# Kernel optimization log

Hardware: AMD Instinct MI355X
Metric: run time of the kernel (lower is better)

The kernel has to match this reference:

```python
import jax, jax.numpy as jnp
import numpy as np
import math

ESM_DIM = 1280

def setup_inputs() -> dict:
    key = jax.random.key(0)
    ks = jax.random.split(key, 12)
    B, Ls, Lc, D = 16, 1024, 2048, ESM_DIM
    scale = 0.02
    return {
        "cyclase": jax.random.normal(ks[0], (B, Lc, D), jnp.float32),
        "substrate": jax.random.normal(ks[1], (B, Ls, D), jnp.float32),
        "cyclase_mask": jnp.ones((B, Lc), jnp.float32),
        "substrate_mask": jnp.ones((B, Ls), jnp.float32),
        "Wq": jax.random.uniform(ks[2], (D, D), jnp.float32) * scale,
        "Wk": jax.random.uniform(ks[3], (D, D), jnp.float32) * scale,
        "Wv": jax.random.uniform(ks[4], (D, D), jnp.float32) * scale,
        "W1": jax.random.normal(ks[5], (2 * D, 512), jnp.float32) * scale,
        "b1": jnp.zeros((512,), jnp.float32),
        "W2": jax.random.normal(ks[6], (512, 64), jnp.float32) * scale,
        "b2": jnp.zeros((64,), jnp.float32),
        "W3": jax.random.normal(ks[7], (64, 1), jnp.float32) * scale,
        "b3": jnp.zeros((1,), jnp.float32),
    }


def reference(cyclase, substrate, cyclase_mask, substrate_mask,
              Wq, Wk, Wv, W1, b1, W2, b2, W3, b3):
    # Cross attention: substrate is the query, cyclase is key/value.
    q = jnp.einsum('bsd,de->bse', substrate, Wq)   # [B,Ls,D]
    k = jnp.einsum('bcd,de->bce', cyclase, Wk)     # [B,Lc,D]
    v = jnp.einsum('bcd,de->bce', cyclase, Wv)     # [B,Lc,D]
    scores = jnp.einsum('bse,bce->bsc', q, k) / math.sqrt(q.shape[-1])
    # NOTE: original torch code masks `attn_scores` but softmaxes
    # `scaled_attn_scores`, so the padding mask has no effect. Replicated.
    weights = jax.nn.softmax(scores, axis=-1)      # [B,Ls,Lc]
    attn_out = jnp.einsum('bsc,bce->bse', weights, v)  # [B,Ls,D]
    x1_avg = jnp.mean(attn_out, axis=1)            # [B,D]
    sub_avg = jnp.mean(substrate, axis=1)          # [B,D]
    x = jnp.concatenate([x1_avg, sub_avg], axis=1) # [B,2D]
    h = jax.nn.relu(x @ W1 + b1)
    h = jax.nn.relu(h @ W2 + b2)
    return jax.nn.sigmoid(h @ W3 + b3)             # [B,1]
```

## Files before the change

### kernel.cpp

```cpp
#include <hip/hip_runtime.h>
#include <hip/hip_bf16.h>

#define DEV static __device__ __forceinline__

typedef __attribute__((ext_vector_type(16))) float f32x16;
typedef __attribute__((ext_vector_type(8)))  short bf16x8;

#if defined(__has_builtin)
#  if __has_builtin(__builtin_amdgcn_cvt_pk_fp8_f32) && __has_builtin(__builtin_amdgcn_cvt_f32_fp8)
#    define HW_FP8 1
#  endif
#endif

DEV ushort f2bf(float f){
  union { float f; unsigned u; } v; v.f = f;
  return (ushort)((v.u + 0x7FFFu + ((v.u >> 16) & 1u)) >> 16);
}
DEV float bf2f(ushort u){
  union { unsigned u; float f; } v; v.u = ((unsigned)u) << 16;
  return v.f;
}

DEV unsigned char f2e4m3_sw(float f){
  union { float f; unsigned u; } v; v.f = f;
  unsigned s = (v.u >> 24) & 0x80;
  float a = fabsf(f);
  if (a >= 448.f) return s | 0x7E;
  if (a < 0.0009765625f) return (unsigned char)s;
  if (a < 0.015625f) {
    int m = (int)rintf(a * 512.f);
    return (unsigned char)(s | (m >= 8 ? 8 : m));
  }
  unsigned ab = v.u & 0x7FFFFFFF;
  unsigned r = ab + 0x0007FFFF + ((ab >> 20) & 1);
  unsigned e = (r >> 23) - 127 + 7;
  unsigned m = (r >> 20) & 7;
  if (e > 15 || (e == 15 && m > 6)) return s | 0x7E;
  return (unsigned char)(s | (e << 3) | m);
}
DEV float e4m32f_sw(unsigned char c){
  unsigned e = (c >> 3) & 15, m = c & 7;
  float v;
  if (e) { union { unsigned u; float f; } w; w.u = ((e + 120u) << 23) | (m << 20); v = w.f; }
  else v = (float)m * 0.001953125f;
  return (c & 0x80) ? -v : v;
}

DEV unsigned pack4_fp8(float a, float b, float c, float d){
#ifdef HW_FP8
  int v = __builtin_amdgcn_cvt_pk_fp8_f32(a, b, 0, false);
  v = __builtin_amdgcn_cvt_pk_fp8_f32(c, d, v, true);
  return (unsigned)v;
#else
  return (unsigned)f2e4m3_sw(a) | ((unsigned)f2e4m3_sw(b) << 8)
       | ((unsigned)f2e4m3_sw(c) << 16) | ((unsigned)f2e4m3_sw(d) << 24);
#endif
}
DEV unsigned char enc_fp8(float a){
#ifdef HW_FP8
  return (unsigned char)(__builtin_amdgcn_cvt_pk_fp8_f32(a, a, 0, false) & 0xFF);
#else
  return f2e4m3_sw(a);
#endif
}
template<int SEL>
DEV float dec_fp8(unsigned u){
#ifdef HW_FP8
  return __builtin_amdgcn_cvt_f32_fp8((int)u, SEL);
#else
  return e4m32f_sw((u >> (SEL * 8)) & 0xFF);
#endif
}

DEV void gload16(const void* g, void* l) {
  __builtin_amdgcn_global_load_lds(
      (const __attribute__((address_space(1))) unsigned*)g,
      (__attribute__((address_space(3))) unsigned*)l, 16, 0, 0);
}

__global__ __launch_bounds__(256)
void cvt_wqk(const float* __restrict__ Wq, const float* __restrict__ Wk,
             ushort* __restrict__ Wq16, ushort* __restrict__ Wk16)
{
  const float* src = blockIdx.y ? Wk : Wq;
  ushort* dst = blockIdx.y ? Wk16 : Wq16;
  const long n8 = 1280l * 1280 / 8;
  const long stride = (long)gridDim.x * 256;
  for (long i = (long)blockIdx.x * 256 + threadIdx.x; i < n8; i += stride) {
    const float4 a = *(const float4*)(src + i * 8);
    const float4 b = *(const float4*)(src + i * 8 + 4);
    union { ushort u[8]; uint4 v; } pk;
    pk.u[0] = f2bf(a.x); pk.u[1] = f2bf(a.y); pk.u[2] = f2bf(a.z); pk.u[3] = f2bf(a.w);
    pk.u[4] = f2bf(b.x); pk.u[5] = f2bf(b.y); pk.u[6] = f2bf(b.z); pk.u[7] = f2bf(b.w);
    *(uint4*)(dst + i * 8) = pk.v;
  }
}

__global__ __launch_bounds__(256)
void cyccvt(const float* __restrict__ cyc, unsigned* __restrict__ cyc8w,
            float* __restrict__ gsum)
{
  const int lane = threadIdx.x & 63, wid = threadIdx.x >> 6;
  const long row = (long)blockIdx.x * 4 + wid;
  const float* src = cyc + row * 1280;
  unsigned* dst = cyc8w + row * 320;
  float s = 0.f;
  #pragma unroll
  for (int i = 0; i < 5; i++) {
    const int d = i * 256 + lane * 4;
    const float4 v = *(const float4*)(src + d);
    s += v.x + v.y + v.z + v.w;
    dst[d >> 2] = pack4_fp8(v.x * 16.f, v.y * 16.f, v.z * 16.f, v.w * 16.f);
  }
  #pragma unroll
  for (int o = 1; o < 64; o <<= 1) s += __shfl_xor(s, o);
  if (lane == 0) gsum[row] = s;
}

__global__ __launch_bounds__(256)
void subprep(const float* __restrict__ sub, const float* __restrict__ mcol,
             unsigned* __restrict__ sub8w, float* __restrict__ tbar)
{
  __shared__ float mc[1280];
  for (int i = threadIdx.x; i < 1280; i += 256) mc[i] = mcol[i];
  __syncthreads();
  const int lane = threadIdx.x & 63, wid = threadIdx.x >> 6;
  const long row = (long)blockIdx.x * 4 + wid;
  const float4* sp = (const float4*)(sub + row * 1280);
  unsigned* dp = sub8w + row * 320;
  float d = 0.f;
  #pragma unroll
  for (int i = 0; i < 5; i++) {
    const int c = i * 64 + lane;
    const float4 v = sp[c];
    d += v.x * mc[c * 4] + v.y * mc[c * 4 + 1] + v.z * mc[c * 4 + 2] + v.w * mc[c * 4 + 3];
    dp[c] = pack4_fp8(v.x * 16.f, v.y * 16.f, v.z * 16.f, v.w * 16.f);
  }
  #pragma unroll
  for (int o = 1; o < 64; o <<= 1) d += __shfl_xor(d, o);
  if (lane == 0) tbar[row] = d;
}

__global__ __launch_bounds__(512, 4)
void gemm_mkq(const ushort* __restrict__ A, const ushort* __restrict__ B,
              ushort* __restrict__ C, int K, int N, int nbx, float scale,
              float* __restrict__ mcol)
{
  __shared__ __align__(16) ushort As[4][4][128][8];
  __shared__ __align__(16) ushort Bs[4][4][128][8];
  const int tid = threadIdx.x, lane = tid & 63, wid = tid >> 6;
  const int wr = wid >> 2, wc = wid & 3;
  const int bx = blockIdx.x % nbx, by = blockIdx.x / nbx;
  const int bm = by * 128, bn = bx * 128;

  f32x16 acc[2];
  #pragma unroll
  for (int i = 0; i < 2; i++)
    #pragma unroll
    for (int e = 0; e < 16; e++) acc[i][e] = 0.f;

  const int kbA = wid >> 1, rqA = wid & 1;
  const ushort* agp = A + (long)(bm + rqA * 64 + lane) * K + kbA * 8;
  const ushort* bgp = B + (long)(bn + rqA * 64 + lane) * K + kbA * 8;
  auto STAGE = [&](int g, int rg) {
    gload16(agp + g * 32, &As[rg][kbA][rqA * 64][0]);
    gload16(bgp + g * 32, &Bs[rg][kbA][rqA * 64][0]);
  };
  const int NG = K >> 5;
  STAGE(0, 0); STAGE(1, 1);
  asm volatile("s_waitcnt vmcnt(2)" ::: "memory");
  __builtin_amdgcn_s_barrier();
  const int lkh = lane >> 5, lr = lane & 31;
  auto GROUP = [&](int g, int rg, int rg2) {
    bf16x8 av[2][2], bv[2];
    #pragma unroll
    for (int kf = 0; kf < 2; kf++) {
      #pragma unroll
      for (int mi = 0; mi < 2; mi++)
        av[mi][kf] = *(const bf16x8*)&As[rg][kf * 2 + lkh][wr * 64 + mi * 32 + lr][0];
      bv[kf] = *(const bf16x8*)&Bs[rg][kf * 2 + lkh][wc * 32 + lr][0];
    }
    if (g + 2 < NG) STAGE(g + 2, rg2);
    __builtin_amdgcn_s_barrier();
    __builtin_amdgcn_s_setprio(1);
    #pragma unroll
    for (int mi = 0; mi < 2; mi++)
      #pragma unroll
      for (int kf = 0; kf < 2; kf++)
        acc[mi] = __builtin_amdgcn_mfma_f32_32x32x16_bf16(av[mi][kf], bv[kf], acc[mi], 0, 0, 0);
    __builtin_amdgcn_s_setprio(0);
    if (g + 2 < NG)      asm volatile("s_waitcnt vmcnt(2)" ::: "memory");
    else if (g + 1 < NG) asm volatile("s_waitcnt vmcnt(0)" ::: "memory");
    __builtin_amdgcn_s_barrier();
  };
  for (int g = 0; g < NG; g += 4) {
    GROUP(g, 0, 2); GROUP(g + 1, 1, 3); GROUP(g + 2, 2, 0); GROUP(g + 3, 3, 1);
  }
  float csum = 0.f;
  #pragma unroll
  for (int mi = 0; mi < 2; mi++)
    #pragma unroll
    for (int rr = 0; rr < 16; rr++) {
      const int row = bm + wr * 64 + mi * 32 + (rr & 3) + 8 * (rr >> 2) + 4 * lkh;
      const int col = bn + wc * 32 + lr;
      const float v = acc[mi][rr] * scale;
      csum += v;
      C[(long)row * N + col] = f2bf(v);
    }
  atomicAdd(&mcol[bn + wc * 32 + lr], csum * (1.f / 1280.f));
}

__global__ __launch_bounds__(320)
void m2cvt(const ushort* __restrict__ Mkq, const float* __restrict__ mcol,
           unsigned* __restrict__ M2w)
{
  const int j = blockIdx.x;
  const int d = threadIdx.x * 4;
  const ushort* mr = Mkq + (long)j * 1280 + d;
  const float* mc = mcol + d;
  M2w[j * 320 + threadIdx.x] = pack4_fp8(
      (bf2f(mr[0]) - mc[0]) * 524288.f, (bf2f(mr[1]) - mc[1]) * 524288.f,
      (bf2f(mr[2]) - mc[2]) * 524288.f, (bf2f(mr[3]) - mc[3]) * 524288.f);
}

template<int MODE, bool BY_FAST>
__global__ __launch_bounds__(512, 2)
void gemm_f8(const unsigned char* __restrict__ A, const unsigned char* __restrict__ B,
             void* __restrict__ Cv, int K, int N, int nbx, int nby,
             long sA, long sB, long sC,
             const float* __restrict__ tbar, const float* __restrict__ gsum)
{
  __shared__ __align__(16) unsigned char As[4][4][256][16];
  __shared__ __align__(16) unsigned char Bs[4][4][256][16];
  const int tid = threadIdx.x, lane = tid & 63, wid = tid >> 6;
  const int wr = wid >> 2, wc = wid & 3;

  const int nwg = gridDim.x;
  const int q = nwg >> 3, r = nwg & 7;
  const int xcd = blockIdx.x & 7, lid = blockIdx.x >> 3;
  const int id = (xcd < r ? xcd * (q + 1) : r * (q + 1) + (xcd - r) * q) + lid;
  const int per = nbx * nby;
  const int z = id / per, rem = id - z * per;
  const int bx = BY_FAST ? rem / nby : rem % nbx;
  const int by = BY_FAST ? rem % nby : rem / nbx;
  const int bm = by * 256, bn = bx * 256;
  const long Ab = (long)z * sA, Bb = (long)z * sB, Cb = (long)z * sC;

  f32x16 acc[4][2];
  #pragma unroll
  for (int i = 0; i < 4; i++)
    #pragma unroll
    for (int j = 0; j < 2; j++)
      #pragma unroll
      for (int e = 0; e < 16; e++) acc[i][j][e] = 0.f;

  const int c0 = wid * 2, c1 = wid * 2 + 1;
  const int kb0 = c0 >> 2, rq0 = c0 & 3, kb1 = c1 >> 2, rq1 = c1 & 3;
  const unsigned char* ag0 = A + Ab + (long)(bm + rq0 * 64 + lane) * K + kb0 * 16;
  const unsigned char* ag1 = A + Ab + (long)(bm + rq1 * 64 + lane) * K + kb1 * 16;
  const unsigned char* bg0 = B + Bb + (long)(bn + rq0 * 64 + lane) * K + kb0 * 16;
  const unsigned char* bg1 = B + Bb + (long)(bn + rq1 * 64 + lane) * K + kb1 * 16;
  auto STAGE_A = [&](int g, int rg) {
    gload16(ag0 + g * 64, &As[rg][kb0][rq0 * 64][0]);
    gload16(ag1 + g * 64, &As[rg][kb1][rq1 * 64][0]);
  };
  auto STAGE_B = [&](int g, int rg) {
    gload16(bg0 + g * 64, &Bs[rg][kb0][rq0 * 64][0]);
    gload16(bg1 + g * 64, &Bs[rg][kb1][rq1 * 64][0]);
  };

  const int NG = K >> 6;
  STAGE_A(0, 0); STAGE_B(0, 0); STAGE_A(1, 1); STAGE_B(1, 1);
  asm volatile("s_waitcnt vmcnt(4)" ::: "memory");
  __builtin_amdgcn_s_barrier();

  const int lkh = lane >> 5, lr = lane & 31;

  auto GROUP = [&](int g, int rg, int rg2) {
    const bool pre = (g + 2 < NG);
    long av[2][4], bv[2][4];
    #pragma unroll
    for (int kf = 0; kf < 4; kf++) {
      #pragma unroll
      for (int mi = 0; mi < 2; mi++)
        av[mi][kf] = *(const long*)&As[rg][kf][wr * 128 + mi * 32 + lr][lkh * 8];
      #pragma unroll
      for (int ni = 0; ni < 2; ni++)
        bv[ni][kf] = *(const long*)&Bs[rg][kf][wc * 64 + ni * 32 + lr][lkh * 8];
    }
    if (pre) STAGE_A(g + 2, rg2);
    __builtin_amdgcn_s_barrier();
    __builtin_amdgcn_s_setprio(1);
    #pragma unroll
    for (int kf = 0; kf < 4; kf++)
      #pragma unroll
      for (int mi = 0; mi < 2; mi++)
        #pragma unroll
        for (int ni = 0; ni < 2; ni++)
          acc[mi][ni] = __builtin_amdgcn_mfma_f32_32x32x16_fp8_fp8(av[mi][kf], bv[ni][kf], acc[mi][ni], 0, 0, 0);
    __builtin_amdgcn_s_setprio(0);
    __builtin_amdgcn_s_barrier();
    #pragma unroll
    for (int kf = 0; kf < 4; kf++)
      #pragma unroll
      for (int mi = 0; mi < 2; mi++)
        av[mi][kf] = *(const long*)&As[rg][kf][wr * 128 + (mi + 2) * 32 + lr][lkh * 8];
    if (pre) STAGE_B(g + 2, rg2);
    __builtin_amdgcn_s_barrier();
    __builtin_amdgcn_s_setprio(1);
    #pragma unroll
    for (int kf = 0; kf < 4; kf++)
      #pragma unroll
      for (int mi = 0; mi < 2; mi++)
        #pragma unroll
        for (int ni = 0; ni < 2; ni++)
          acc[mi + 2][ni] = __builtin_amdgcn_mfma_f32_32x32x16_fp8_fp8(av[mi][kf], bv[ni][kf], acc[mi + 2][ni], 0, 0, 0);
    __builtin_amdgcn_s_setprio(0);
    if (pre)             asm volatile("s_waitcnt vmcnt(4)" ::: "memory");
    else if (g + 1 < NG) asm volatile("s_waitcnt vmcnt(0)" ::: "memory");
    __builtin_amdgcn_s_barrier();
  };

  for (int g = 0; g < NG; g += 4) {
    GROUP(g, 0, 2); GROUP(g + 1, 1, 3); GROUP(g + 2, 2, 0); GROUP(g + 3, 3, 1);
  }

  #pragma unroll
  for (int mi = 0; mi < 4; mi++)
    #pragma unroll
    for (int ni = 0; ni < 2; ni++)
      #pragma unroll
      for (int rr = 0; rr < 16; rr++) {
        const int row = bm + wr * 128 + mi * 32 + (rr & 3) + 8 * (rr >> 2) + 4 * lkh;
        const int col = bn + wc * 64 + ni * 32 + lr;
        if constexpr (MODE == 0) {
          const float v = acc[mi][ni][rr] * 0x1p-16f
                        + tbar[(long)z * 1024 + row] * gsum[(long)z * 2048 + col];
          ((ushort*)Cv)[Cb + (long)row * N + col] = f2bf(v);
        } else {
          ((unsigned char*)Cv)[Cb + (long)row * N + col] = enc_fp8(acc[mi][ni][rr] * 0x1p-11f);
        }
      }
}

__global__ __launch_bounds__(512, 4)
void gemm_f8_128(const unsigned char* __restrict__ A, const unsigned char* __restrict__ B,
                 unsigned char* __restrict__ C, int K, int N, int nbx)
{
  __shared__ __align__(16) unsigned char As[4][4][128][16];
  __shared__ __align__(16) unsigned char Bs[4][4][128][16];
  const int tid = threadIdx.x, lane = tid & 63, wid = tid >> 6;
  const int wr = wid >> 2, wc = wid & 3;

  const int nwg = gridDim.x;
  const int q = nwg >> 3, r = nwg & 7;
  const int xcd = blockIdx.x & 7, lid = blockIdx.x >> 3;
  const int id = (xcd < r ? xcd * (q + 1) : r * (q + 1) + (xcd - r) * q) + lid;
  const int bx = id % nbx, by = id / nbx;
  const int bm = by * 128, bn = bx * 128;

  f32x16 acc[2];
  #pragma unroll
  for (int i = 0; i < 2; i++)
    #pragma unroll
    for (int e = 0; e < 16; e++) acc[i][e] = 0.f;

  const int kbA = wid >> 1, rhA = wid & 1;
  const unsigned char* agp = A + (long)(bm + rhA * 64 + lane) * K + kbA * 16;
  const unsigned char* bgp = B + (long)(bn + rhA * 64 + lane) * K + kbA * 16;
  auto STAGE = [&](int g, int rg) {
    gload16(agp + g * 64, &As[rg][kbA][rhA * 64][0]);
    gload16(bgp + g * 64, &Bs[rg][kbA][rhA * 64][0]);
  };
  const int NG = K >> 6;
  STAGE(0, 0); STAGE(1, 1);
  asm volatile("s_waitcnt vmcnt(2)" ::: "memory");
  __builtin_amdgcn_s_barrier();

  const int lkh = lane >> 5, lr = lane & 31;

  auto GROUP = [&](int g, int rg, int rg2) {
    long av[2][4], bv[4];
    #pragma unroll
    for (int kf = 0; kf < 4; kf++) {
      #pragma unroll
      for (int mi = 0; mi < 2; mi++)
        av[mi][kf] = *(const long*)&As[rg][kf][wr * 64 + mi * 32 + lr][lkh * 8];
      bv[kf] = *(const long*)&Bs[rg][kf][wc * 32 + lr][lkh * 8];
    }
    if (g + 2 < NG) STAGE(g + 2, rg2);
    __builtin_amdgcn_s_barrier();
    __builtin_amdgcn_s_setprio(1);
    #pragma unroll
    for (int kf = 0; kf < 4; kf++)
      #pragma unroll
      for (int mi = 0; mi < 2; mi++)
        acc[mi] = __builtin_amdgcn_mfma_f32_32x32x16_fp8_fp8(av[mi][kf], bv[kf], acc[mi], 0, 0, 0);
    __builtin_amdgcn_s_setprio(0);
    if (g + 2 < NG)      asm volatile("s_waitcnt vmcnt(2)" ::: "memory");
    else if (g + 1 < NG) asm volatile("s_waitcnt vmcnt(0)" ::: "memory");
    __builtin_amdgcn_s_barrier();
  };
  for (int g = 0; g < NG; g += 4) {
    GROUP(g, 0, 2); GROUP(g + 1, 1, 3); GROUP(g + 2, 2, 0); GROUP(g + 3, 3, 1);
  }

  #pragma unroll
  for (int mi = 0; mi < 2; mi++)
    #pragma unroll
    for (int rr = 0; rr < 16; rr++) {
      const int row = bm + wr * 64 + mi * 32 + (rr & 3) + 8 * (rr >> 2) + 4 * lkh;
      const int col = bn + wc * 32 + lr;
      C[(long)row * N + col] = enc_fp8(acc[mi][rr] * 0x1p-11f);
    }
}

__global__ __launch_bounds__(256)
void softmax_wsum(const ushort* __restrict__ S, float* __restrict__ wsum)
{
  const int b = blockIdx.x;
  const int s0 = blockIdx.y * 16;
  const int lane = threadIdx.x & 63;
  const int w = threadIdx.x >> 6;
  __shared__ float red[4][2048];
  const ushort* Sb = S + (((long)b * 1024) + s0 + w * 4) * 2048;

  float acc[32];
  #pragma unroll
  for (int i = 0; i < 32; i++) acc[i] = 0.f;
  for (int r = 0; r < 4; r++) {
    const ushort* row = Sb + (long)r * 2048;
    float v[32];
    #pragma unroll
    for (int i = 0; i < 4; i++) {
      uint4 u = *(const uint4*)(row + i * 512 + lane * 8);
      const ushort* up = (const ushort*)&u;
      #pragma unroll
      for (int j = 0; j < 8; j++) v[i * 8 + j] = bf2f(up[j]);
    }
    float m = v[0];
    #pragma unroll
    for (int i = 1; i < 32; i++) m = fmaxf(m, v[i]);
    #pragma unroll
    for (int o = 1; o < 64; o <<= 1) m = fmaxf(m, __shfl_xor(m, o));
    float ssum = 0.f;
    #pragma unroll
    for (int i = 0; i < 32; i++) { v[i] = __expf(v[i] - m); ssum += v[i]; }
    #pragma unroll
    for (int o = 1; o < 64; o <<= 1) ssum += __shfl_xor(ssum, o);
    const float inv = 1.f / ssum;
    #pragma unroll
    for (int i = 0; i < 32; i++) acc[i] += v[i] * inv;
  }
  #pragma unroll
  for (int i = 0; i < 4; i++)
    #pragma unroll
    for (int j = 0; j < 8; j++)
      red[w][i * 512 + lane * 8 + j] = acc[i * 8 + j];
  __syncthreads();
  float* wb = wsum + b * 2048;
  #pragma unroll
  for (int k = 0; k < 8; k++) {
    const int c = k * 256 + threadIdx.x;
    atomicAdd(&wb[c], red[0][c] + red[1][c] + red[2][c] + red[3][c]);
  }
}

__global__ __launch_bounds__(320)
void wcyc_kernel(const unsigned char* __restrict__ cyc8, const float* __restrict__ wsum,
                 float* __restrict__ t)
{
  const int b = blockIdx.x;
  const int c0 = blockIdx.y * 64;
  const int d = threadIdx.x * 4;
  const unsigned char* cb = cyc8 + ((long)b * 2048 + c0) * 1280 + d;
  const float* wb = wsum + b * 2048 + c0;
  float4 a = {0.f, 0.f, 0.f, 0.f};
  for (int c = 0; c < 64; c++) {
    const unsigned u = *(const unsigned*)(cb + (long)c * 1280);
    const float w = wb[c];
    a.x += w * dec_fp8<0>(u); a.y += w * dec_fp8<1>(u);
    a.z += w * dec_fp8<2>(u); a.w += w * dec_fp8<3>(u);
  }
  atomicAdd(&t[b * 1280 + d + 0], a.x * 0.0625f);
  atomicAdd(&t[b * 1280 + d + 1], a.y * 0.0625f);
  atomicAdd(&t[b * 1280 + d + 2], a.z * 0.0625f);
  atomicAdd(&t[b * 1280 + d + 3], a.w * 0.0625f);
}

__global__ __launch_bounds__(320)
void submean8(const unsigned char* __restrict__ sub8, float* __restrict__ xcat)
{
  const int b = blockIdx.x;
  const int s0 = blockIdx.y * 64;
  const int d = threadIdx.x * 4;
  const unsigned char* sp = sub8 + ((long)b * 1024 + s0) * 1280 + d;
  float4 a = {0.f, 0.f, 0.f, 0.f};
  for (int s = 0; s < 64; s++) {
    const unsigned u = *(const unsigned*)(sp + (long)s * 1280);
    a.x += dec_fp8<0>(u); a.y += dec_fp8<1>(u);
    a.z += dec_fp8<2>(u); a.w += dec_fp8<3>(u);
  }
  const float k = 1.f / (16.f * 1024.f);
  atomicAdd(&xcat[b * 2560 + 1280 + d + 0], a.x * k);
  atomicAdd(&xcat[b * 2560 + 1280 + d + 1], a.y * k);
  atomicAdd(&xcat[b * 2560 + 1280 + d + 2], a.z * k);
  atomicAdd(&xcat[b * 2560 + 1280 + d + 3], a.w * k);
}

__global__ __launch_bounds__(256)
void xv_fused(const float* __restrict__ t, const float* __restrict__ Wv,
              float* __restrict__ xcat)
{
  const int dp0 = blockIdx.x * 64;
  const int d0 = blockIdx.y * 256;
  __shared__ float tl[16 * 256];
  __shared__ float red[4][64][16];
  for (int i = threadIdx.x; i < 16 * 256; i += 256) {
    const int b = i >> 8, d = i & 255;
    tl[i] = t[b * 1280 + d0 + d];
  }
  __syncthreads();
  const int dpi = threadIdx.x & 63;
  const int grp = threadIdx.x >> 6;
  float acc[16];
  #pragma unroll
  for (int b = 0; b < 16; b++) acc[b] = 0.f;
  for (int dd = 0; dd < 64; dd++) {
    const int d = grp * 64 + dd;
    const float w = Wv[(long)(d0 + d) * 1280 + dp0 + dpi];
    #pragma unroll
    for (int b = 0; b < 16; b++) acc[b] += w * tl[b * 256 + d];
  }
  #pragma unroll
  for (int b = 0; b < 16; b++) red[grp][dpi][b] = acc[b];
  __syncthreads();
  #pragma unroll
  for (int k = 0; k < 4; k++) {
    const int o = k * 256 + threadIdx.x;
    const int dp = o >> 4, b = o & 15;
    const float v = red[0][dp][b] + red[1][dp][b] + red[2][dp][b] + red[3][dp][b];
    atomicAdd(&xcat[b * 2560 + dp0 + dp], v * (1.f / 1024.f));
  }
}

__global__ __launch_bounds__(256)
void mlp1_fused(const float* __restrict__ xcat, const float* __restrict__ W1,
                float* __restrict__ h1pre)
{
  const int j0 = blockIdx.x * 64;
  const int d0 = blockIdx.y * 320;
  __shared__ float xl[16 * 320];
  __shared__ float red[4][64][16];
  for (int i = threadIdx.x; i < 16 * 320; i += 256) {
    const int b = i / 320, d = i % 320;
    xl[i] = xcat[b * 2560 + d0 + d];
  }
  __syncthreads();
  const int ji = threadIdx.x & 63;
  const int grp = threadIdx.x >> 6;
  float acc[16];
  #pragma unroll
  for (int b = 0; b < 16; b++) acc[b] = 0.f;
  for (int dd = 0; dd < 80; dd++) {
    const int d = grp * 80 + dd;
    const float w = W1[(long)(d0 + d) * 512 + j0 + ji];
    #pragma unroll
    for (int b = 0; b < 16; b++) acc[b] += w * xl[b * 320 + d];
  }
  #pragma unroll
  for (int b = 0; b < 16; b++) red[grp][ji][b] = acc[b];
  __syncthreads();
  #pragma unroll
  for (int k = 0; k < 4; k++) {
    const int o = k * 256 + threadIdx.x;
    const int j = o >> 4, b = o & 15;
    const float v = red[0][j][b] + red[1][j][b] + red[2][j][b] + red[3][j][b];
    atomicAdd(&h1pre[b * 512 + j0 + j], v);
  }
}

__global__ __launch_bounds__(64)
void mlp23_kernel(const float* __restrict__ h1pre, const float* __restrict__ b1,
                  const float* __restrict__ W2, const float* __restrict__ b2,
                  const float* __restrict__ W3, const float* __restrict__ b3,
                  float* __restrict__ out)
{
  const int b = blockIdx.x;
  const int j = threadIdx.x;
  __shared__ float hl[512];
  for (int i = j; i < 512; i += 64) hl[i] = fmaxf(h1pre[b * 512 + i] + b1[i], 0.f);
  __syncthreads();
  float a = b2[j];
  for (int d = 0; d < 512; d++) a += hl[d] * W2[d * 64 + j];
  a = fmaxf(a, 0.f);
  float p = a * W3[j];
  #pragma unroll
  for (int o = 1; o < 64; o <<= 1) p += __shfl_xor(p, o);
  if (j == 0) out[b] = 1.f / (1.f + __expf(-(p + b3[0])));
}

extern "C" void kernel_launch(void* const* d_in, const int* in_sizes, int n_in,
                              void* d_out, int out_size, void* d_ws, size_t ws_size,
                              hipStream_t stream)
{
  const float* cyclase   = (const float*)d_in[0];
  const float* substrate = (const float*)d_in[1];
  const float* Wq = (const float*)d_in[4];
  const float* Wk = (const float*)d_in[5];
  const float* Wv = (const float*)d_in[6];
  const float* W1 = (const float*)d_in[7];
  const float* b1 = (const float*)d_in[8];
  const float* W2 = (const float*)d_in[9];
  const float* b2 = (const float*)d_in[10];
  const float* W3 = (const float*)d_in[11];
  const float* b3 = (const float*)d_in[12];
  float* out = (float*)d_out;
  (void)in_sizes; (void)n_in; (void)out_size; (void)ws_size;

  char* ws = (char*)d_ws;
  unsigned char* cyc8 = (unsigned char*)ws;
  char* A2 = ws + 41943040;
  ushort* Mkq   = (ushort*)(A2 + 41943040);
  ushort* Wq16  = (ushort*)(A2 + 41943040 + 3276800);
  ushort* Wk16  = (ushort*)(A2 + 41943040 + 2 * 3276800);
  unsigned char* sub8 = (unsigned char*)(A2 + 41943040 + 3 * 3276800);
  ushort* S = (ushort*)A2;
  char* B2 = A2 + 41943040 + 3 * 3276800 + 20971520;
  unsigned char* T1p8 = (unsigned char*)B2;
  unsigned char* M2_8 = (unsigned char*)(B2 + 20971520);
  char* C2 = B2 + 20971520 + 1638400;
  float* mcol  = (float*)C2;
  float* tbar  = (float*)(C2 + 8192);
  float* gsum  = (float*)(C2 + 8192 + 65536);
  float* wsum  = (float*)(C2 + 8192 + 65536 + 131072);
  float* tbuf  = (float*)(C2 + 8192 + 65536 + 2 * 131072);
  float* xcat  = (float*)(C2 + 8192 + 65536 + 2 * 131072 + 81920);
  float* h1pre = (float*)(C2 + 8192 + 65536 + 2 * 131072 + 81920 + 163840);

  hipMemsetAsync(C2, 0, 8192 + 65536 + 2 * 131072 + 81920 + 163840 + 32768, stream);

  cvt_wqk<<<dim3(200, 2), 256, 0, stream>>>(Wq, Wk, Wq16, Wk16);
  cyccvt<<<8192, 256, 0, stream>>>(cyclase, (unsigned*)cyc8, gsum);

  gemm_mkq<<<100, 512, 0, stream>>>(Wk16, Wq16, Mkq, 1280, 1280, 10,
                                    0.02795084971874737f, mcol);
  m2cvt<<<1280, 320, 0, stream>>>(Mkq, mcol, (unsigned*)M2_8);

  subprep<<<4096, 256, 0, stream>>>(substrate, mcol, (unsigned*)sub8, tbar);
  submean8<<<dim3(16, 16), 320, 0, stream>>>(sub8, xcat);

  gemm_f8_128<<<1280, 512, 0, stream>>>(sub8, M2_8, T1p8, 1280, 1280, 10);

  gemm_f8<0, true><<<512, 512, 0, stream>>>(T1p8, cyc8, S,
      1280, 2048, 8, 4, 1024l * 1280, 2048l * 1280, 1024l * 2048, tbar, gsum);

  softmax_wsum<<<dim3(16, 64), 256, 0, stream>>>(S, wsum);
  wcyc_kernel<<<dim3(16, 32), 320, 0, stream>>>(cyc8, wsum, tbuf);
  xv_fused<<<dim3(20, 5), 256, 0, stream>>>(tbuf, Wv, xcat);
  mlp1_fused<<<dim3(8, 8), 256, 0, stream>>>(xcat, W1, h1pre);
  mlp23_kernel<<<16, 64, 0, stream>>>(h1pre, b1, W2, b2, W3, b3, out);
}
```

Measured before the change: 368.2 us.

## Split score GEMM 256x256 tile across 16 waves instead of 8

The batched score GEMM now runs with 1024 threads per block. Each of 16 waves computes a 64x64 sub-tile, where before 8 waves each computed 128x64. Each wave issues one A and one B 16-byte load per stage, and the two-phase compute with its extra barrier per k-group is collapsed into a single phase. This is meant to raise wave-level parallelism and latency hiding while halving per-thread accumulator registers. In exchange, barriers now synchronise twice as many waves, and the launch bound of 4 may be unattainable given the LDS tile size.

```diff
diff --git a/kernel.cpp b/kernel.cpp
--- a/kernel.cpp
+++ b/kernel.cpp
@@ -223,12 +223,11 @@
       (bf2f(mr[2]) - mc[2]) * 524288.f, (bf2f(mr[3]) - mc[3]) * 524288.f);
 }
 
-template<int MODE, bool BY_FAST>
-__global__ __launch_bounds__(512, 2)
-void gemm_f8(const unsigned char* __restrict__ A, const unsigned char* __restrict__ B,
-             void* __restrict__ Cv, int K, int N, int nbx, int nby,
-             long sA, long sB, long sC,
-             const float* __restrict__ tbar, const float* __restrict__ gsum)
+__global__ __launch_bounds__(1024, 4)
+void gemm_f8_s(const unsigned char* __restrict__ A, const unsigned char* __restrict__ B,
+               ushort* __restrict__ C, int K, int N, int nbx, int nby,
+               long sA, long sB, long sC,
+               const float* __restrict__ tbar, const float* __restrict__ gsum)
 {
   __shared__ __align__(16) unsigned char As[4][4][256][16];
   __shared__ __align__(16) unsigned char Bs[4][4][256][16];
@@ -241,54 +240,45 @@
   const int id = (xcd < r ? xcd * (q + 1) : r * (q + 1) + (xcd - r) * q) + lid;
   const int per = nbx * nby;
   const int z = id / per, rem = id - z * per;
-  const int bx = BY_FAST ? rem / nby : rem % nbx;
-  const int by = BY_FAST ? rem % nby : rem / nbx;
+  const int bx = rem / nby, by = rem % nby;
   const int bm = by * 256, bn = bx * 256;
   const long Ab = (long)z * sA, Bb = (long)z * sB, Cb = (long)z * sC;
 
-  f32x16 acc[4][2];
-  #pragma unroll
-  for (int i = 0; i < 4; i++)
+  f32x16 acc[2][2];
+  #pragma unroll
+  for (int i = 0; i < 2; i++)
     #pragma unroll
     for (int j = 0; j < 2; j++)
       #pragma unroll
       for (int e = 0; e < 16; e++) acc[i][j][e] = 0.f;
 
-  const int c0 = wid * 2, c1 = wid * 2 + 1;
-  const int kb0 = c0 >> 2, rq0 = c0 & 3, kb1 = c1 >> 2, rq1 = c1 & 3;
-  const unsigned char* ag0 = A + Ab + (long)(bm + rq0 * 64 + lane) * K + kb0 * 16;
-  const unsigned char* ag1 = A + Ab + (long)(bm + rq1 * 64 + lane) * K + kb1 * 16;
-  const unsigned char* bg0 = B + Bb + (long)(bn + rq0 * 64 + lane) * K + kb0 * 16;
-  const unsigned char* bg1 = B + Bb + (long)(bn + rq1 * 64 + lane) * K + kb1 * 16;
-  auto STAGE_A = [&](int g, int rg) {
-    gload16(ag0 + g * 64, &As[rg][kb0][rq0 * 64][0]);
-    gload16(ag1 + g * 64, &As[rg][kb1][rq1 * 64][0]);
+  const int kbW = wid >> 2, rqW = wid & 3;
+  const unsigned char* agp = A + Ab + (long)(bm + rqW * 64 + lane) * K + kbW * 16;
+  const unsigned char* bgp = B + Bb + (long)(bn + rqW * 64 + lane) * K + kbW * 16;
+  auto STAGE = [&](int g, int rg) {
+    gload16(agp + g * 64, &As[rg][kbW][rqW * 64][0]);
+    gload16(bgp + g * 64, &Bs[rg][kbW][rqW * 64][0]);
   };
-  auto STAGE_B = [&](int g, int rg) {
-    gload16(bg0 + g * 64, &Bs[rg][kb0][rq0 * 64][0]);
-    gload16(bg1 + g * 64, &Bs[rg][kb1][rq1 * 64][0]);
-  };
 
   const int NG = K >> 6;
-  STAGE_A(0, 0); STAGE_B(0, 0); STAGE_A(1, 1); STAGE_B(1, 1);
-  asm volatile("s_waitcnt vmcnt(4)" ::: "memory");
+  STAGE(0, 0); STAGE(1, 1);
+  asm volatile("s_waitcnt vmcnt(2)" ::: "memory");
   __builtin_amdgcn_s_barrier();
 
   const int lkh = lane >> 5, lr = lane & 31;
 
   auto GROUP = [&](int g, int rg, int rg2) {
-    const bool pre = (g + 2 < NG);
     long av[2][4], bv[2][4];
     #pragma unroll
     for (int kf = 0; kf < 4; kf++) {
       #pragma unroll
       for (int mi = 0; mi < 2; mi++)
-        av[mi][kf] = *(const long*)&As[rg][kf][wr * 128 + mi * 32 + lr][lkh * 8];
+        av[mi][kf] = *(const long*)&As[rg][kf][wr * 64 + mi * 32 + lr][lkh * 8];
       #pragma unroll
       for (int ni = 0; ni < 2; ni++)
         bv[ni][kf] = *(const long*)&Bs[rg][kf][wc * 64 + ni * 32 + lr][lkh * 8];
     }
-    if (pre) STAGE_A(g + 2, rg2);
+    if (g + 2 < NG) STAGE(g + 2, rg2);
     __builtin_amdgcn_s_barrier();
     __builtin_amdgcn_s_setprio(1);
     #pragma unroll
@@ -299,24 +289,7 @@
         for (int ni = 0; ni < 2; ni++)
           acc[mi][ni] = __builtin_amdgcn_mfma_f32_32x32x16_fp8_fp8(av[mi][kf], bv[ni][kf], acc[mi][ni], 0, 0, 0);
     __builtin_amdgcn_s_setprio(0);
-    __builtin_amdgcn_s_barrier();
-    #pragma unroll
-    for (int kf = 0; kf < 4; kf++)
-      #pragma unroll
-      for (int mi = 0; mi < 2; mi++)
-        av[mi][kf] = *(const long*)&As[rg][kf][wr * 128 + (mi + 2) * 32 + lr][lkh * 8];
-    if (pre) STAGE_B(g + 2, rg2);
-    __builtin_amdgcn_s_barrier();
-    __builtin_amdgcn_s_setprio(1);
-    #pragma unroll
-    for (int kf = 0; kf < 4; kf++)
-      #pragma unroll
-      for (int mi = 0; mi < 2; mi++)
-        #pragma unroll
-        for (int ni = 0; ni < 2; ni++)
-          acc[mi + 2][ni] = __builtin_amdgcn_mfma_f32_32x32x16_fp8_fp8(av[mi][kf], bv[ni][kf], acc[mi + 2][ni], 0, 0, 0);
-    __builtin_amdgcn_s_setprio(0);
-    if (pre)             asm volatile("s_waitcnt vmcnt(4)" ::: "memory");
+    if (g + 2 < NG)      asm volatile("s_waitcnt vmcnt(2)" ::: "memory");
     else if (g + 1 < NG) asm volatile("s_waitcnt vmcnt(0)" ::: "memory");
     __builtin_amdgcn_s_barrier();
   };
@@ -326,20 +299,16 @@
   }
 
   #pragma unroll
-  for (int mi = 0; mi < 4; mi++)
+  for (int mi = 0; mi < 2; mi++)
     #pragma unroll
     for (int ni = 0; ni < 2; ni++)
       #pragma unroll
       for (int rr = 0; rr < 16; rr++) {
-        const int row = bm + wr * 128 + mi * 32 + (rr & 3) + 8 * (rr >> 2) + 4 * lkh;
+        const int row = bm + wr * 64 + mi * 32 + (rr & 3) + 8 * (rr >> 2) + 4 * lkh;
         const int col = bn + wc * 64 + ni * 32 + lr;
-        if constexpr (MODE == 0) {
-          const float v = acc[mi][ni][rr] * 0x1p-16f
-                        + tbar[(long)z * 1024 + row] * gsum[(long)z * 2048 + col];
-          ((ushort*)Cv)[Cb + (long)row * N + col] = f2bf(v);
-        } else {
-          ((unsigned char*)Cv)[Cb + (long)row * N + col] = enc_fp8(acc[mi][ni][rr] * 0x1p-11f);
-        }
+        const float v = acc[mi][ni][rr] * 0x1p-16f
+                      + tbar[(long)z * 1024 + row] * gsum[(long)z * 2048 + col];
+        C[Cb + (long)row * N + col] = f2bf(v);
       }
 }
 
@@ -652,7 +621,7 @@
 
   gemm_f8_128<<<1280, 512, 0, stream>>>(sub8, M2_8, T1p8, 1280, 1280, 10);
 
-  gemm_f8<0, true><<<512, 512, 0, stream>>>(T1p8, cyc8, S,
+  gemm_f8_s<<<512, 1024, 0, stream>>>(T1p8, cyc8, S,
       1280, 2048, 8, 4, 1024l * 1280, 2048l * 1280, 1024l * 2048, tbar, gsum);
 
   softmax_wsum<<<dim3(16, 64), 256, 0, stream>>>(S, wsum);
```

After: 393.1 us. 6.8% more time.
